# Kernel optimization log

Measured on AMD Instinct MI355X. Metric: run time of the kernel, lower is better.

The kernel has to match this reference:

```python
import jax, jax.numpy as jnp
import numpy as np

NUM_GROUPS = 32
EPS = 1e-6


def group_norm(x, gamma, beta):
    # x: [b, c, h, w]
    b, c, h, w = x.shape
    g = NUM_GROUPS
    xg = x.reshape(b, g, c // g, h, w)
    mean = jnp.mean(xg, axis=(2, 3, 4), keepdims=True)
    var = jnp.var(xg, axis=(2, 3, 4), keepdims=True)
    xg = (xg - mean) * jax.lax.rsqrt(var + EPS)
    x = xg.reshape(b, c, h, w)
    return x * gamma[None, :, None, None] + beta[None, :, None, None]


def conv1x1(x, w, bias):
    # x: [b, c_in, h, w], w: [c_out, c_in], bias: [c_out]
    return jnp.einsum('bihw,oi->bohw', x, w) + bias[None, :, None, None]


def setup_inputs() -> dict:
    key = jax.random.key(0)
    ks = jax.random.split(key, 10)
    c = 512
    b, h, w = 4, 64, 64
    scale = 1.0 / np.sqrt(c)
    inp = {
        'x': jax.random.normal(ks[0], (b, c, h, w), dtype=jnp.float32),
        'gn_gamma': jnp.ones((c,), dtype=jnp.float32),
        'gn_beta': jnp.zeros((c,), dtype=jnp.float32),
        'wq': jax.random.normal(ks[1], (c, c), dtype=jnp.float32) * scale,
        'bq': jnp.zeros((c,), dtype=jnp.float32),
        'wk': jax.random.normal(ks[2], (c, c), dtype=jnp.float32) * scale,
        'bk': jnp.zeros((c,), dtype=jnp.float32),
        'wv': jax.random.normal(ks[3], (c, c), dtype=jnp.float32) * scale,
        'bv': jnp.zeros((c,), dtype=jnp.float32),
        'wo': jax.random.normal(ks[4], (c, c), dtype=jnp.float32) * scale,
        'bo': jnp.zeros((c,), dtype=jnp.float32),
    }
    return inp


def reference(x, gn_gamma, gn_beta, wq, bq, wk, bk, wv, bv, wo, bo):
    b, c, h, w = x.shape
    h_ = group_norm(x, gn_gamma, gn_beta)
    q = conv1x1(h_, wq, bq)
    k = conv1x1(h_, wk, bk)
    v = conv1x1(h_, wv, bv)
    n = h * w
    q = q.reshape(b, c, n).transpose(0, 2, 1)  # [b, n, c]
    k = k.reshape(b, c, n)                      # [b, c, n]
    v = v.reshape(b, c, n).transpose(0, 2, 1)  # [b, n, c]
    sim = jnp.einsum('bqc,bck->bqk', q, k) * (c ** -0.5)  # [b, n, n]
    attn = jax.nn.softmax(sim, axis=-1)
    out = jnp.einsum('bqk,bkc->bqc', attn, v)  # [b, n, c]
    out = out.transpose(0, 2, 1).reshape(b, c, h, w)
    out = conv1x1(out, wo, bo)
    return x + out
```

## Files before the change

kernel.cpp:

```cpp
#include <hip/hip_runtime.h>


typedef __attribute__((ext_vector_type(8))) short bf16x8;
typedef __attribute__((ext_vector_type(4))) float f32x4;

#define MFMA16(a, b, c) __builtin_amdgcn_mfma_f32_16x16x32_bf16((a), (b), (c), 0, 0, 0)

#define B_   4
#define C_   512
#define N_   4096
#define SCALE 0.044194173824159216f
#define ESHIFT 12.0f
#define SC2   0.06376297465050853f
#define ES2   17.312340490667562f

__device__ __forceinline__ unsigned short f2bf(float f) {
    union { float f; unsigned int u; } v; v.f = f;
    unsigned int r = (v.u + 0x7fffu + ((v.u >> 16) & 1u)) >> 16;
    return (unsigned short)r;
}
__device__ __forceinline__ float bf2f(unsigned short s) {
    union { unsigned int u; float f; } v; v.u = ((unsigned int)s) << 16;
    return v.f;
}
// ... 26 lines not shown
    if (t == 0) { part[blk] = red[0]; part[512 + blk] = red[256]; }
}

__global__ __launch_bounds__(256) void gn_apply(const float* __restrict__ x,
                                                const float* __restrict__ gamma,
                                                const float* __restrict__ beta,
                                                const float* __restrict__ part,
                                                unsigned short* __restrict__ ht) {
    __shared__ float tile[64][65];
    __shared__ float mrs[4][2];
    int j0 = blockIdx.x * 64, c0 = blockIdx.y * 64, b = blockIdx.z;
    int t = threadIdx.x;
    if (t < 4) {
        int gid = b * 32 + (c0 >> 4) + t;
        float s = 0.f, ss = 0.f;
#pragma unroll
        for (int q = 0; q < 4; ++q) { s += part[gid * 4 + q]; ss += part[512 + gid * 4 + q]; }
        float mean = s * (1.f / 65536.f);
        float var  = ss * (1.f / 65536.f) - mean * mean;
        mrs[t][0] = mean;
        mrs[t][1] = rsqrtf(var + 1e-6f);
    }
    __syncthreads();
#pragma unroll
    for (int i = 0; i < 16; ++i) {
        int lid = i * 256 + t;
        int cl = lid >> 6, jl = lid & 63;
        int c = c0 + cl;
        float v = x[((size_t)b * C_ + c) * N_ + j0 + jl];
        tile[cl][jl] = (v - mrs[cl >> 4][0]) * mrs[cl >> 4][1] * gamma[c] + beta[c];
    }
    __syncthreads();
#pragma unroll
    for (int i = 0; i < 16; ++i) {
        int lid = i * 256 + t;
        int jl = lid >> 6, cl = lid & 63;
        ht[((size_t)b * N_ + j0 + jl) * C_ + c0 + cl] = f2bf(tile[cl][jl]);
    }
}

__global__ __launch_bounds__(256) void wconv(const float* __restrict__ wq,
                                             const float* __restrict__ wk,
                                             const float* __restrict__ wv,
                                             const float* __restrict__ wo,
                                             unsigned short* __restrict__ dst) {
    size_t i = (size_t)blockIdx.x * 256 + threadIdx.x;
    int m = (int)(i >> 18);
    size_t off = i & 262143;
    const float* src = (m == 0) ? wq : (m == 1) ? wk : (m == 2) ? wv : wo;
    dst[i] = f2bf(src[off]);
}

template <typename EPI>
__device__ __forceinline__ void gemm_core(const unsigned short* __restrict__ Abase,
                                          const unsigned short* __restrict__ Bbase,
                                          size_t lda, size_t ldb, int K, EPI epi) {
    __shared__ unsigned short hl[2][128 * 64];
    __shared__ unsigned short wl[2][128 * 64];
    int t = threadIdx.x;
    int wv = t >> 6, lane = t & 63, l15 = lane & 15, quad = lane >> 4;
    int wm = wv & 1, wn = wv >> 1;
    int srow = lane >> 3;
    int sch  = ((lane & 7) ^ srow) * 8;
    int xr = l15 & 7;
    f32x4 acc[4][4] = {};
#pragma unroll
    for (int i = 0; i < 4; ++i) {
        int seg = wv * 4 + i;
        size_t row = seg * 8 + srow;
        async16(&Abase[row * lda + sch], &hl[0][seg * 512]);
        async16(&Bbase[row * ldb + sch], &wl[0][seg * 512]);
    }
    int nk = K >> 6;
    for (int k = 0; k < nk; ++k) {
        int cur = k & 1;
        __builtin_amdgcn_s_waitcnt(0x3F70);
        __syncthreads();
        if (k + 1 < nk) {
            int k0 = (k + 1) << 6;
#pragma unroll
            for (int i = 0; i < 4; ++i) {
                int seg = wv * 4 + i;
                size_t row = seg * 8 + srow;
                async16(&Abase[row * lda + k0 + sch], &hl[cur ^ 1][seg * 512]);
                async16(&Bbase[row * ldb + k0 + sch], &wl[cur ^ 1][seg * 512]);
            }
        }
#pragma unroll
        for (int kk = 0; kk < 2; ++kk) {
            int sl = (((kk << 2) + quad) ^ xr) * 8;
            bf16x8 af[4], bfr[4];
#pragma unroll
            for (int mi = 0; mi < 4; ++mi)
                af[mi] = *(const bf16x8*)&hl[cur][(wm * 64 + mi * 16 + l15) * 64 + sl];
#pragma unroll
            for (int ni = 0; ni < 4; ++ni)
                bfr[ni] = *(const bf16x8*)&wl[cur][(wn * 64 + ni * 16 + l15) * 64 + sl];
#pragma unroll
            for (int mi = 0; mi < 4; ++mi)
#pragma unroll
                for (int ni = 0; ni < 4; ++ni)
                    acc[mi][ni] = MFMA16(af[mi], bfr[ni], acc[mi][ni]);
        }
    }
    epi(acc, wm, wn, l15, quad);
}

__global__ __launch_bounds__(256) void gemm_qkv(const unsigned short* __restrict__ Ht,
                                                const unsigned short* __restrict__ Wb,
                                                const float* __restrict__ bq,
                                                const float* __restrict__ bk,
                                                const float* __restrict__ bv,
                                                unsigned short* __restrict__ Qt,
                                                unsigned short* __restrict__ Kt,
                                                unsigned short* __restrict__ Vg) {
    int b = blockIdx.z, j0 = blockIdx.x * 128;
    int ct = blockIdx.y;
    int slab = ct >> 2, co0 = (ct & 3) * 128;
    const unsigned short* A = Ht + ((size_t)b * N_ + j0) * C_;
    const unsigned short* B = Wb + (size_t)slab * C_ * C_ + (size_t)co0 * C_;
    const float* bias = (slab == 0) ? bq : (slab == 1) ? bk : bv;
    unsigned short* outqk = (slab == 0) ? Qt : Kt;
    gemm_core(A, B, C_, C_, C_,
        [&](f32x4 (&acc)[4][4], int wm, int wn, int l15, int quad) {
        if (slab < 2) {
#pragma unroll
            for (int mi = 0; mi < 4; ++mi)
#pragma unroll
                for (int ni = 0; ni < 4; ++ni)
#pragma unroll
                    for (int r = 0; r < 4; ++r) {
                        int mrow = wm * 64 + mi * 16 + quad * 4 + r;
                        int ncol = wn * 64 + ni * 16 + l15;
                        outqk[((size_t)b * N_ + j0 + mrow) * C_ + co0 + ncol] =
                            f2bf(acc[mi][ni][r] + bias[co0 + ncol]);
                    }
        } else {
#pragma unroll
            for (int mi = 0; mi < 4; ++mi)
#pragma unroll
                for (int ni = 0; ni < 4; ++ni) {
                    int ncol = wn * 64 + ni * 16 + l15;
                    float bb = bias[co0 + ncol];
                    ushort4 pk;
                    pk.x = f2bf(acc[mi][ni][0] + bb);
                    pk.y = f2bf(acc[mi][ni][1] + bb);
                    pk.z = f2bf(acc[mi][ni][2] + bb);
                    pk.w = f2bf(acc[mi][ni][3] + bb);
                    int jb = j0 + wm * 64 + mi * 16 + quad * 4;
                    *(ushort4*)&Vg[((size_t)b * C_ + co0 + ncol) * N_ + jb] = pk;
                }
        }
    });
}

__global__ __launch_bounds__(512, 4) void gemm_qk_exp(const unsigned short* __restrict__ Qt,
                                                      const unsigned short* __restrict__ Kt,
                                                      unsigned short* __restrict__ P,
                                                      float* __restrict__ psum) {
    extern __shared__ unsigned short sm[];
    int lin = blockIdx.x;
    int xcd = lin & 7;
    int i   = lin >> 3;
    int rid = xcd + 8 * (i >> 4);
    int idx = i & 15;
    int mi4 = idx & 1, ni4 = idx >> 1;
    int b   = rid >> 5;
    int rem = rid & 31;
    int rm  = rem & 7, rn = rem >> 3;
    int j0  = (rm * 2 + mi4) * 256;
    int ky  = rn * 8 + ni4;
    int kc0 = ky * 128;
    const unsigned short* A  = Qt + ((size_t)b * N_ + j0) * C_;
    const unsigned short* Bm = Kt + ((size_t)b * N_ + kc0) * C_;

    int t = threadIdx.x;
    int w = t >> 6, lane = t & 63, l15 = lane & 15, quad = lane >> 4;
    int wm = w >> 1, wn = w & 1;
    int srow = lane >> 2;
    int sch  = ((lane & 3) ^ ((lane >> 3) & 3)) * 8;
    int slotq = (quad ^ ((l15 >> 1) & 3)) * 8;

    const unsigned short* gA0 = A + ((size_t)(w * 2 + 0) * 16 + srow) * C_ + sch;
    const unsigned short* gA1 = A + ((size_t)(w * 2 + 1) * 16 + srow) * C_ + sch;
    const unsigned short* gB  = Bm + ((size_t)w * 16 + srow) * C_ + sch;

    f32x4 acc[4][4] = {};
    const int NT = 16;
    unsigned short* bA = sm;
    unsigned short* bB = sm + 12288;
    unsigned short* bC = sm + 24576;

    async16(gA0,      bA + (w * 2 + 0) * 512);
    async16(gA1,      bA + (w * 2 + 1) * 512);
    async16(gB,       bA + 8192 + w * 512);
    async16(gA0 + 32, bB + (w * 2 + 0) * 512);
    async16(gA1 + 32, bB + (w * 2 + 1) * 512);
    async16(gB  + 32, bB + 8192 + w * 512);
    gA0 += 64; gA1 += 64; gB += 64;
    __builtin_amdgcn_s_waitcnt(0x3F73);
    __builtin_amdgcn_s_barrier();

    for (int tt = 0; tt < NT; ++tt) {
        if (tt + 2 < NT) {
            async16(gA0, bC + (w * 2 + 0) * 512);
            async16(gA1, bC + (w * 2 + 1) * 512);
            async16(gB,  bC + 8192 + w * 512);
            gA0 += 32; gA1 += 32; gB += 32;
        }
        bf16x8 af[4], bfr[4];
#pragma unroll
        for (int mi = 0; mi < 4; ++mi)
            af[mi] = *(const bf16x8*)&bA[(wm * 64 + mi * 16 + l15) * 32 + slotq];
#pragma unroll
        for (int ni = 0; ni < 4; ++ni)
            bfr[ni] = *(const bf16x8*)&bA[8192 + (wn * 64 + ni * 16 + l15) * 32 + slotq];
        __builtin_amdgcn_s_setprio(1);
#pragma unroll
        for (int mi = 0; mi < 4; ++mi)
#pragma unroll
            for (int ni = 0; ni < 4; ++ni)
                acc[mi][ni] = MFMA16(af[mi], bfr[ni], acc[mi][ni]);
        __builtin_amdgcn_s_setprio(0);
        if (tt + 1 < NT) {
            if (tt + 2 < NT) __builtin_amdgcn_s_waitcnt(0x3F73);
            else             __builtin_amdgcn_s_waitcnt(0x3F70);
            __builtin_amdgcn_s_barrier();
        }
        unsigned short* tmp = bA; bA = bB; bB = bC; bC = tmp;
    }

#pragma unroll
    for (int mi = 0; mi < 4; ++mi) {
        float rs[4] = {0.f, 0.f, 0.f, 0.f};
#pragma unroll
        for (int ni = 0; ni < 4; ++ni) {
            int ncol = kc0 + wn * 64 + ni * 16 + l15;
#pragma unroll
            for (int r = 0; r < 4; ++r) {
                int mrow = j0 + wm * 64 + mi * 16 + quad * 4 + r;
                float p = exp2f(__builtin_fmaf(acc[mi][ni][r], SC2, -ES2));
                rs[r] += p;
                P[((size_t)b * N_ + mrow) * N_ + ncol] = f2bf(p);
            }
        }
#pragma unroll
        for (int r = 0; r < 4; ++r) {
            float v = rs[r];
            v += __shfl_xor(v, 1);
            v += __shfl_xor(v, 2);
            v += __shfl_xor(v, 4);
            v += __shfl_xor(v, 8);
            if (l15 == 0)
                psum[(size_t)(ky * 2 + wn) * 16384 +
                     (size_t)b * N_ + j0 + wm * 64 + mi * 16 + quad * 4 + r] = v;
        }
    }
}

__global__ __launch_bounds__(512, 2) void gemm_pv(const unsigned short* __restrict__ P,
                                                  const unsigned short* __restrict__ Vg,
                                                  const float* __restrict__ psum,
                                                  unsigned short* __restrict__ ao) {
    extern __shared__ unsigned short sm[];
    __shared__ float linv[256];
    int lin = blockIdx.x;
    int xcd = lin & 7;
    int i4  = lin >> 3;
    int ct  = i4 & 3;
    int grp = xcd + 8 * (i4 >> 2);
    int b = grp & 3, qtile = grp >> 2;
    int j0 = qtile * 256, co0 = ct * 128;
    int t = threadIdx.x;
    int w = t >> 6, lane = t & 63, l15 = lane & 15, quad = lane >> 4;
    int wm = w >> 1, wn = w & 1;
    int srow = lane >> 2;
    int sch  = ((lane & 3) ^ ((lane >> 3) & 3)) * 8;
    int slotq = (quad ^ ((l15 >> 1) & 3)) * 8;
    const unsigned short* A  = P  + ((size_t)b * N_ + j0) * N_;
    const unsigned short* Bm = Vg + ((size_t)b * C_ + co0) * N_;
    f32x4 acc[4][4] = {};
    const int NT = 128;
#pragma unroll
    for (int tt = 0; tt < 2; ++tt) {
        unsigned short* dst = sm + tt * 12288;
        size_t k0 = (size_t)tt << 5;
#pragma unroll
        for (int i = 0; i < 2; ++i) {
            int seg = w * 2 + i;
            size_t row = (size_t)seg * 16 + srow;
            async16(&A[row * N_ + k0 + sch], dst + seg * 512);
        }
        {
            size_t row = (size_t)w * 16 + srow;
            async16(&Bm[row * N_ + k0 + sch], dst + 8192 + w * 512);
        }
    }
    if (t < 256) {
        size_t q = (size_t)b * N_ + j0 + t;
        float s = 0.f;
#pragma unroll
        for (int i = 0; i < 64; ++i) s += psum[(size_t)i * 16384 + q];
        linv[t] = 1.f / s;
    }
    __builtin_amdgcn_s_waitcnt(0x3F73);
    __builtin_amdgcn_s_barrier();
    for (int tt = 0; tt < NT; tt += 2) {
#pragma unroll
        for (int s = 0; s < 2; ++s) {
            int tc = tt + s;
// ... 2 lines not shown
            bf16x8 af[4], bfr[4];
#pragma unroll
            for (int mi = 0; mi < 4; ++mi)
                af[mi] = *(const bf16x8*)&bp[(wm * 64 + mi * 16 + l15) * 32 + slotq];
#pragma unroll
            for (int ni = 0; ni < 4; ++ni)
                bfr[ni] = *(const bf16x8*)&bp[8192 + (wn * 64 + ni * 16 + l15) * 32 + slotq];
            if (ts < NT) {
                unsigned short* stg = sm + (ts & 3) * 12288;
                size_t k0n = (size_t)ts << 5;
#pragma unroll
                for (int i = 0; i < 2; ++i) {
                    int seg = w * 2 + i;
                    size_t row = (size_t)seg * 16 + srow;
                    async16(&A[row * N_ + k0n + sch], stg + seg * 512);
                }
                {
                    size_t row = (size_t)w * 16 + srow;
                    async16(&Bm[row * N_ + k0n + sch], stg + 8192 + w * 512);
                }
            }
            __builtin_amdgcn_s_setprio(1);
#pragma unroll
            for (int mi = 0; mi < 4; ++mi)
#pragma unroll
                for (int ni = 0; ni < 4; ++ni)
                    acc[mi][ni] = MFMA16(af[mi], bfr[ni], acc[mi][ni]);
            __builtin_amdgcn_s_setprio(0);
            if (s == 0) {
                if (tt + 2 < NT) __builtin_amdgcn_s_waitcnt(0x3F73);
                else             __builtin_amdgcn_s_waitcnt(0x3F70);
                __builtin_amdgcn_sched_barrier(0);
            }
        }
        if (tt + 2 < NT) {
            if (tt + 3 < NT) __builtin_amdgcn_s_waitcnt(0x3F73);
            else             __builtin_amdgcn_s_waitcnt(0x3F70);
            __builtin_amdgcn_s_barrier();
        }
    }
#pragma unroll
    for (int mi = 0; mi < 4; ++mi)
#pragma unroll
        for (int ni = 0; ni < 4; ++ni)
#pragma unroll
            for (int r = 0; r < 4; ++r) {
                int mrow = wm * 64 + mi * 16 + quad * 4 + r;
                int ncol = wn * 64 + ni * 16 + l15;
                ao[((size_t)b * N_ + j0 + mrow) * C_ + co0 + ncol] =
                    f2bf(acc[mi][ni][r] * linv[mrow]);
            }
}

__global__ __launch_bounds__(256) void gemm_resid(const unsigned short* __restrict__ AObf,
                                                  const unsigned short* __restrict__ Wo,
                                                  const float* __restrict__ bo,
                                                  const float* __restrict__ xres,
                                                  float* __restrict__ out) {
    int b = blockIdx.z, j0 = blockIdx.x * 128, co0 = blockIdx.y * 128;
    const unsigned short* A = AObf + ((size_t)b * N_ + j0) * C_;
    const unsigned short* B = Wo + (size_t)co0 * C_;
    gemm_core(A, B, C_, C_, C_,
        [&](f32x4 (&acc)[4][4], int wm, int wn, int l15, int quad) {
#pragma unroll
        for (int mi = 0; mi < 4; ++mi)
#pragma unroll
            for (int ni = 0; ni < 4; ++ni) {
                int ncol = wn * 64 + ni * 16 + l15;
                int jb = j0 + wm * 64 + mi * 16 + quad * 4;
                size_t o = ((size_t)b * C_ + co0 + ncol) * N_ + jb;
                float bb = bo[co0 + ncol];
                float4 xr = *(const float4*)&xres[o];
                float4 ov;
                ov.x = acc[mi][ni][0] + bb + xr.x;
                ov.y = acc[mi][ni][1] + bb + xr.y;
                ov.z = acc[mi][ni][2] + bb + xr.z;
                ov.w = acc[mi][ni][3] + bb + xr.w;
                *(float4*)&out[o] = ov;
            }
    });
}

__global__ __launch_bounds__(256, 1) void flash_attn(const unsigned short* __restrict__ Qt,
                                                     const unsigned short* __restrict__ Kt,
                                                     const unsigned short* __restrict__ Vg,
                                                     unsigned short* __restrict__ part,
                                                     float* __restrict__ lbuf,
                                                     int nsplit) {
    extern __shared__ unsigned short smem[];
    unsigned short* Kl = smem;
    unsigned short* Vl = smem + 32768;
    unsigned short* Pl = smem + 65536;

    int flat = blockIdx.x;
    int qblk, b, s;
    if (nsplit == 2) { s = flat & 1; b = (flat >> 1) & 3; qblk = flat >> 3; }
    else             { s = 0;        b = flat & 3;        qblk = flat >> 2; }
    int q0 = qblk * 128;
    int t = threadIdx.x, w = t >> 6, lane = t & 63, l15 = lane & 15, quad = lane >> 4;
    int klen = N_ / nsplit, kbeg = s * klen, nkt = klen / 32;
    int xr = l15 & 7;

    const unsigned short* Kbase = Kt + (size_t)b * N_ * C_;
    const unsigned short* Vbase = Vg + (size_t)b * C_ * N_;

    bf16x8 qa[2][16];
// ... 122 lines not shown
    size_t row = idx >> 6;
    float l = lbuf[row];
    union { uint4 v; unsigned short u[8]; } p1, p2, outv;
    p1.v = *(const uint4*)&part[row * C_ + cu * 8];
    if (nsplit == 2) {
        l += lbuf[(size_t)B_ * N_ + row];
        p2.v = *(const uint4*)&part[((size_t)B_ * N_ + row) * C_ + cu * 8];
    } else {
        p2.v = make_uint4(0, 0, 0, 0);
    }
    float inv = 1.f / l;
#pragma unroll
    for (int j = 0; j < 8; ++j)
        outv.u[j] = f2bf((bf2f(p1.u[j]) + bf2f(p2.u[j])) * inv);
    *(uint4*)&ao[row * C_ + cu * 8] = outv.v;
}

extern "C" void kernel_launch(void* const* d_in, const int* in_sizes, int n_in,
                              void* d_out, int out_size, void* d_ws, size_t ws_size,
                              hipStream_t stream) {
    const float* x   = (const float*)d_in[0];
    const float* gam = (const float*)d_in[1];
    const float* bet = (const float*)d_in[2];
    const float* wq  = (const float*)d_in[3];
    const float* bq  = (const float*)d_in[4];
    const float* wk  = (const float*)d_in[5];
    const float* bk  = (const float*)d_in[6];
    const float* wv  = (const float*)d_in[7];
    const float* bv  = (const float*)d_in[8];
    const float* wo  = (const float*)d_in[9];
    const float* bo  = (const float*)d_in[10];
    float* out = (float*)d_out;

    char* ws = (char*)d_ws;
    const size_t SZH = (size_t)B_ * N_ * C_ * 2;
    const size_t OFF_HT = 4096;
    const size_t OFF_QT = OFF_HT + SZH;
    const size_t OFF_KT = OFF_QT + SZH;
    const size_t OFF_VG = OFF_KT + SZH;
    const size_t OFF_WB = OFF_VG + SZH;
    const size_t OFF_X  = OFF_WB + 2097152;
    float*          part0 = (float*)ws;
    unsigned short* Ht    = (unsigned short*)(ws + OFF_HT);
    unsigned short* Qt    = (unsigned short*)(ws + OFF_QT);
    unsigned short* Kt    = (unsigned short*)(ws + OFF_KT);
    unsigned short* Vg    = (unsigned short*)(ws + OFF_VG);
    unsigned short* Wb    = (unsigned short*)(ws + OFF_WB);
    unsigned short* AObf  = Ht;

    const size_t SZPSUM = 64ull * 16384 * 4;
    const size_t SZP    = (size_t)B_ * N_ * N_ * 2;
    float*          psum = (float*)(ws + OFF_X);
    unsigned short* P    = (unsigned short*)(ws + OFF_X + SZPSUM);
    size_t needA = OFF_X + SZPSUM + SZP;

    float*          lbuf = (float*)(ws + OFF_X);
    unsigned short* partb = (unsigned short*)(ws + OFF_X + 262144);
    size_t needB2 = OFF_X + 262144 + 2 * SZH;

    gn_partial<<<512, 256, 0, stream>>>(x, part0);
    gn_apply<<<dim3(64, 8, B_), 256, 0, stream>>>(x, gam, bet, part0, Ht);
    wconv<<<4096, 256, 0, stream>>>(wq, wk, wv, wo, Wb);
    gemm_qkv<<<dim3(32, 12, B_), 256, 0, stream>>>(Ht, Wb, bq, bk, bv, Qt, Kt, Vg);

    if (ws_size >= needA) {
        const int QK_LDS = 73728;
        (void)hipFuncSetAttribute((const void*)gemm_qk_exp,
                                  hipFuncAttributeMaxDynamicSharedMemorySize, QK_LDS);
        gemm_qk_exp<<<2048, 512, QK_LDS, stream>>>(Qt, Kt, P, psum);
        const int PV_LDS = 98304;
        (void)hipFuncSetAttribute((const void*)gemm_pv,
                                  hipFuncAttributeMaxDynamicSharedMemorySize, PV_LDS);
        gemm_pv<<<256, 512, PV_LDS, stream>>>(P, Vg, psum, AObf);
    } else {
        int nsplit = (ws_size >= needB2) ? 2 : 1;
        const int FLASH_LDS = 140288;
        (void)hipFuncSetAttribute((const void*)flash_attn,
                                  hipFuncAttributeMaxDynamicSharedMemorySize, FLASH_LDS);
        flash_attn<<<dim3(32 * B_ * nsplit), 256, FLASH_LDS, stream>>>(Qt, Kt, Vg, partb, lbuf, nsplit);
        attn_combine<<<4096, 256, 0, stream>>>(partb, lbuf, AObf, nsplit);
    }
    gemm_resid<<<dim3(32, 4, B_), 256, 0, stream>>>(AObf, Wb + 786432, bo, x, out);
}
```

Baseline: 320.2 us.

## Factor lean triple-buffered GEMM core; use it for QKV and split-K PV

Moves the triple-buffered 256x128 GEMM pipeline from the QK kernel into a shared lean_core helper. The QKV projection now runs on it as a 768-block, 512-thread kernel. PV attention becomes a two-way split-K: partial fp32 outputs are written to workspace, then combined with a separately computed row inverse sum, which raises block count from 256 to 512 for better CU occupancy. The cost is an extra 64MB fp32 partial buffer round trip and two more kernel launches, and the new PV path is used only when the workspace is large enough.

```diff
diff --git a/kernel.cpp b/kernel.cpp
--- a/kernel.cpp
+++ b/kernel.cpp
@@ -102,76 +102,87 @@
 }
 
 template <typename EPI>
-__device__ __forceinline__ void gemm_core(const unsigned short* __restrict__ Abase,
-                                          const unsigned short* __restrict__ Bbase,
-                                          size_t lda, size_t ldb, int K, EPI epi) {
-    __shared__ unsigned short hl[2][128 * 64];
-    __shared__ unsigned short wl[2][128 * 64];
+__device__ __forceinline__ void lean_core(const unsigned short* __restrict__ A,
+                                          const unsigned short* __restrict__ Bm,
+                                          size_t lda, size_t ldb, int NT,
+                                          unsigned short* sm, EPI epi) {
     int t = threadIdx.x;
-    int wv = t >> 6, lane = t & 63, l15 = lane & 15, quad = lane >> 4;
-    int wm = wv & 1, wn = wv >> 1;
-    int srow = lane >> 3;
-    int sch  = ((lane & 7) ^ srow) * 8;
-    int xr = l15 & 7;
+    int w = t >> 6, lane = t & 63, l15 = lane & 15, quad = lane >> 4;
+    int wm = w >> 1, wn = w & 1;
+    int srow = lane >> 2;
+    int sch  = ((lane & 3) ^ ((lane >> 3) & 3)) * 8;
+    int slotq = (quad ^ ((l15 >> 1) & 3)) * 8;
+
+    const unsigned short* gA0 = A + ((size_t)(w * 2 + 0) * 16 + srow) * lda + sch;
+    const unsigned short* gA1 = A + ((size_t)(w * 2 + 1) * 16 + srow) * lda + sch;
+    const unsigned short* gB  = Bm + ((size_t)w * 16 + srow) * ldb + sch;
+
     f32x4 acc[4][4] = {};
-#pragma unroll
-    for (int i = 0; i < 4; ++i) {
-        int seg = wv * 4 + i;
-        size_t row = seg * 8 + srow;
-        async16(&Abase[row * lda + sch], &hl[0][seg * 512]);
-        async16(&Bbase[row * ldb + sch], &wl[0][seg * 512]);
-    }
-    int nk = K >> 6;
-    for (int k = 0; k < nk; ++k) {
-        int cur = k & 1;
-        __builtin_amdgcn_s_waitcnt(0x3F70);
-        __syncthreads();
-        if (k + 1 < nk) {
-            int k0 = (k + 1) << 6;
-#pragma unroll
-            for (int i = 0; i < 4; ++i) {
-                int seg = wv * 4 + i;
-                size_t row = seg * 8 + srow;
-                async16(&Abase[row * lda + k0 + sch], &hl[cur ^ 1][seg * 512]);
-                async16(&Bbase[row * ldb + k0 + sch], &wl[cur ^ 1][seg * 512]);
-            }
-        }
-#pragma unroll
-        for (int kk = 0; kk < 2; ++kk) {
-            int sl = (((kk << 2) + quad) ^ xr) * 8;
-            bf16x8 af[4], bfr[4];
-#pragma unroll
-            for (int mi = 0; mi < 4; ++mi)
-                af[mi] = *(const bf16x8*)&hl[cur][(wm * 64 + mi * 16 + l15) * 64 + sl];
+    unsigned short* bA = sm;
+    unsigned short* bB = sm + 12288;
+    unsigned short* bC = sm + 24576;
+
+    async16(gA0,      bA + (w * 2 + 0) * 512);
+    async16(gA1,      bA + (w * 2 + 1) * 512);
+    async16(gB,       bA + 8192 + w * 512);
+    async16(gA0 + 32, bB + (w * 2 + 0) * 512);
+    async16(gA1 + 32, bB + (w * 2 + 1) * 512);
+    async16(gB  + 32, bB + 8192 + w * 512);
+    gA0 += 64; gA1 += 64; gB += 64;
+    __builtin_amdgcn_s_waitcnt(0x3F73);
+    __builtin_amdgcn_s_barrier();
+
+    for (int tt = 0; tt < NT; ++tt) {
+        if (tt + 2 < NT) {
+            async16(gA0, bC + (w * 2 + 0) * 512);
+            async16(gA1, bC + (w * 2 + 1) * 512);
+            async16(gB,  bC + 8192 + w * 512);
+            gA0 += 32; gA1 += 32; gB += 32;
+        }
+        bf16x8 af[4], bfr[4];
+#pragma unroll
+        for (int mi = 0; mi < 4; ++mi)
+            af[mi] = *(const bf16x8*)&bA[(wm * 64 + mi * 16 + l15) * 32 + slotq];
+#pragma unroll
+        for (int ni = 0; ni < 4; ++ni)
+            bfr[ni] = *(const bf16x8*)&bA[8192 + (wn * 64 + ni * 16 + l15) * 32 + slotq];
+        __builtin_amdgcn_s_setprio(1);
+#pragma unroll
+        for (int mi = 0; mi < 4; ++mi)
 #pragma unroll
             for (int ni = 0; ni < 4; ++ni)
-                bfr[ni] = *(const bf16x8*)&wl[cur][(wn * 64 + ni * 16 + l15) * 64 + sl];
-#pragma unroll
-            for (int mi = 0; mi < 4; ++mi)
-#pragma unroll
-                for (int ni = 0; ni < 4; ++ni)
-                    acc[mi][ni] = MFMA16(af[mi], bfr[ni], acc[mi][ni]);
-        }
+                acc[mi][ni] = MFMA16(af[mi], bfr[ni], acc[mi][ni]);
+        __builtin_amdgcn_s_setprio(0);
+        if (tt + 1 < NT) {
+            if (tt + 2 < NT) __builtin_amdgcn_s_waitcnt(0x3F73);
+            else             __builtin_amdgcn_s_waitcnt(0x3F70);
+            __builtin_amdgcn_s_barrier();
+        }
+        unsigned short* tmp = bA; bA = bB; bB = bC; bC = tmp;
     }
     epi(acc, wm, wn, l15, quad);
 }
 
-__global__ __launch_bounds__(256) void gemm_qkv(const unsigned short* __restrict__ Ht,
-                                                const unsigned short* __restrict__ Wb,
-                                                const float* __restrict__ bq,
-                                                const float* __restrict__ bk,
-                                                const float* __restrict__ bv,
-                                                unsigned short* __restrict__ Qt,
-                                                unsigned short* __restrict__ Kt,
-                                                unsigned short* __restrict__ Vg) {
-    int b = blockIdx.z, j0 = blockIdx.x * 128;
-    int ct = blockIdx.y;
-    int slab = ct >> 2, co0 = (ct & 3) * 128;
+__global__ __launch_bounds__(512, 4) void gemm_qkv2(const unsigned short* __restrict__ Ht,
+                                                    const unsigned short* __restrict__ Wb,
+                                                    const float* __restrict__ bq,
+                                                    const float* __restrict__ bk,
+                                                    const float* __restrict__ bv,
+                                                    unsigned short* __restrict__ Qt,
+                                                    unsigned short* __restrict__ Kt,
+                                                    unsigned short* __restrict__ Vg) {
+    extern __shared__ unsigned short sm[];
+    int lin = blockIdx.x;
+    int slab = lin % 3;
+    int q    = lin / 3;
+    int b  = q & 3;
+    int ct = (q >> 2) & 3, jt = q >> 4;
+    int j0 = jt * 256, co0 = ct * 128;
     const unsigned short* A = Ht + ((size_t)b * N_ + j0) * C_;
     const unsigned short* B = Wb + (size_t)slab * C_ * C_ + (size_t)co0 * C_;
     const float* bias = (slab == 0) ? bq : (slab == 1) ? bk : bv;
     unsigned short* outqk = (slab == 0) ? Qt : Kt;
-    gemm_core(A, B, C_, C_, C_,
+    lean_core(A, B, C_, C_, 16, sm,
         [&](f32x4 (&acc)[4][4], int wm, int wn, int l15, int quad) {
         if (slab < 2) {
 #pragma unroll
@@ -223,89 +234,89 @@
     int kc0 = ky * 128;
     const unsigned short* A  = Qt + ((size_t)b * N_ + j0) * C_;
     const unsigned short* Bm = Kt + ((size_t)b * N_ + kc0) * C_;
-
-    int t = threadIdx.x;
-    int w = t >> 6, lane = t & 63, l15 = lane & 15, quad = lane >> 4;
-    int wm = w >> 1, wn = w & 1;
-    int srow = lane >> 2;
-    int sch  = ((lane & 3) ^ ((lane >> 3) & 3)) * 8;
-    int slotq = (quad ^ ((l15 >> 1) & 3)) * 8;
-
-    const unsigned short* gA0 = A + ((size_t)(w * 2 + 0) * 16 + srow) * C_ + sch;
-    const unsigned short* gA1 = A + ((size_t)(w * 2 + 1) * 16 + srow) * C_ + sch;
-    const unsigned short* gB  = Bm + ((size_t)w * 16 + srow) * C_ + sch;
-
-    f32x4 acc[4][4] = {};
-    const int NT = 16;
-    unsigned short* bA = sm;
-    unsigned short* bB = sm + 12288;
-    unsigned short* bC = sm + 24576;
-
-    async16(gA0,      bA + (w * 2 + 0) * 512);
-    async16(gA1,      bA + (w * 2 + 1) * 512);
-    async16(gB,       bA + 8192 + w * 512);
-    async16(gA0 + 32, bB + (w * 2 + 0) * 512);
-    async16(gA1 + 32, bB + (w * 2 + 1) * 512);
-    async16(gB  + 32, bB + 8192 + w * 512);
-    gA0 += 64; gA1 += 64; gB += 64;
-    __builtin_amdgcn_s_waitcnt(0x3F73);
-    __builtin_amdgcn_s_barrier();
-
-    for (int tt = 0; tt < NT; ++tt) {
-        if (tt + 2 < NT) {
-            async16(gA0, bC + (w * 2 + 0) * 512);
-            async16(gA1, bC + (w * 2 + 1) * 512);
-            async16(gB,  bC + 8192 + w * 512);
-            gA0 += 32; gA1 += 32; gB += 32;
-        }
-        bf16x8 af[4], bfr[4];
+    lean_core(A, Bm, C_, C_, 16, sm,
+        [&](f32x4 (&acc)[4][4], int wm, int wn, int l15, int quad) {
+#pragma unroll
+        for (int mi = 0; mi < 4; ++mi) {
+            float rs[4] = {0.f, 0.f, 0.f, 0.f};
+#pragma unroll
+            for (int ni = 0; ni < 4; ++ni) {
+                int ncol = kc0 + wn * 64 + ni * 16 + l15;
+#pragma unroll
+                for (int r = 0; r < 4; ++r) {
+                    int mrow = j0 + wm * 64 + mi * 16 + quad * 4 + r;
+                    float p = exp2f(__builtin_fmaf(acc[mi][ni][r], SC2, -ES2));
+                    rs[r] += p;
+                    P[((size_t)b * N_ + mrow) * N_ + ncol] = f2bf(p);
+                }
+            }
+#pragma unroll
+            for (int r = 0; r < 4; ++r) {
+                float v = rs[r];
+                v += __shfl_xor(v, 1);
+                v += __shfl_xor(v, 2);
+                v += __shfl_xor(v, 4);
+                v += __shfl_xor(v, 8);
+                if (l15 == 0)
+                    psum[(size_t)(ky * 2 + wn) * 16384 +
+                         (size_t)b * N_ + j0 + wm * 64 + mi * 16 + quad * 4 + r] = v;
+            }
+        }
+    });
+}
+
+__global__ __launch_bounds__(512, 4) void pv_part(const unsigned short* __restrict__ P,
+                                                  const unsigned short* __restrict__ Vg,
+                                                  float* __restrict__ opart) {
+    extern __shared__ unsigned short sm[];
+    int lin = blockIdx.x;
+    int ks  = lin >> 8;
+    int r   = lin & 255;
+    int b = r & 3, qtile = (r >> 2) & 15, ct = r >> 6;
+    int j0 = qtile * 256, co0 = ct * 128;
+    const unsigned short* A  = P  + ((size_t)b * N_ + j0) * N_ + (size_t)ks * 2048;
+    const unsigned short* Bm = Vg + ((size_t)b * C_ + co0) * N_ + (size_t)ks * 2048;
+    lean_core(A, Bm, N_, N_, 64, sm,
+        [&](f32x4 (&acc)[4][4], int wm, int wn, int l15, int quad) {
 #pragma unroll
         for (int mi = 0; mi < 4; ++mi)
-            af[mi] = *(const bf16x8*)&bA[(wm * 64 + mi * 16 + l15) * 32 + slotq];
-#pragma unroll
-        for (int ni = 0; ni < 4; ++ni)
-            bfr[ni] = *(const bf16x8*)&bA[8192 + (wn * 64 + ni * 16 + l15) * 32 + slotq];
-        __builtin_amdgcn_s_setprio(1);
-#pragma unroll
-        for (int mi = 0; mi < 4; ++mi)
 #pragma unroll
             for (int ni = 0; ni < 4; ++ni)
-                acc[mi][ni] = MFMA16(af[mi], bfr[ni], acc[mi][ni]);
-        __builtin_amdgcn_s_setprio(0);
-        if (tt + 1 < NT) {
-            if (tt + 2 < NT) __builtin_amdgcn_s_waitcnt(0x3F73);
-            else             __builtin_amdgcn_s_waitcnt(0x3F70);
-            __builtin_amdgcn_s_barrier();
-        }
-        unsigned short* tmp = bA; bA = bB; bB = bC; bC = tmp;
-    }
-
-#pragma unroll
-    for (int mi = 0; mi < 4; ++mi) {
-        float rs[4] = {0.f, 0.f, 0.f, 0.f};
-#pragma unroll
-        for (int ni = 0; ni < 4; ++ni) {
-            int ncol = kc0 + wn * 64 + ni * 16 + l15;
-#pragma unroll
-            for (int r = 0; r < 4; ++r) {
-                int mrow = j0 + wm * 64 + mi * 16 + quad * 4 + r;
-                float p = exp2f(__builtin_fmaf(acc[mi][ni][r], SC2, -ES2));
-                rs[r] += p;
-                P[((size_t)b * N_ + mrow) * N_ + ncol] = f2bf(p);
-            }
-        }
-#pragma unroll
-        for (int r = 0; r < 4; ++r) {
-            float v = rs[r];
-            v += __shfl_xor(v, 1);
-            v += __shfl_xor(v, 2);
-            v += __shfl_xor(v, 4);
-            v += __shfl_xor(v, 8);
-            if (l15 == 0)
-                psum[(size_t)(ky * 2 + wn) * 16384 +
-                     (size_t)b * N_ + j0 + wm * 64 + mi * 16 + quad * 4 + r] = v;
-        }
-    }
+#pragma unroll
+                for (int r2 = 0; r2 < 4; ++r2) {
+                    int mrow = wm * 64 + mi * 16 + quad * 4 + r2;
+                    int ncol = wn * 64 + ni * 16 + l15;
+                    opart[((size_t)ks * 16384 + (size_t)b * N_ + j0 + mrow) * C_ +
+                          co0 + ncol] = acc[mi][ni][r2];
+                }
+    });
+}
+
+__global__ __launch_bounds__(256) void pv_linv(const float* __restrict__ psum,
+                                               float* __restrict__ linv) {
+    int q = blockIdx.x * 256 + threadIdx.x;
+    float s = 0.f;
+#pragma unroll
+    for (int i = 0; i < 64; ++i) s += psum[(size_t)i * 16384 + q];
+    linv[q] = 1.f / s;
+}
+
+__global__ __launch_bounds__(256) void pv_comb(const float* __restrict__ part,
+                                               const float* __restrict__ linv,
+                                               unsigned short* __restrict__ ao) {
+    size_t idx = (size_t)blockIdx.x * 256 + threadIdx.x;
+    size_t row = idx >> 7;
+    int c4 = (int)(idx & 127) * 4;
+    size_t o = row * C_ + c4;
+    float4 p0 = *(const float4*)&part[o];
+    float4 p1 = *(const float4*)&part[(size_t)16384 * C_ + o];
+    float inv = linv[row];
+    ushort4 rv;
+    rv.x = f2bf((p0.x + p1.x) * inv);
+    rv.y = f2bf((p0.y + p1.y) * inv);
+    rv.z = f2bf((p0.z + p1.z) * inv);
+    rv.w = f2bf((p0.w + p1.w) * inv);
+    *(ushort4*)&ao[o] = rv;
 }
 
 __global__ __launch_bounds__(512, 2) void gemm_pv(const unsigned short* __restrict__ P,
@@ -414,6 +425,61 @@
             }
 }
 
+template <typename EPI>
+__device__ __forceinline__ void gemm_core(const unsigned short* __restrict__ Abase,
+                                          const unsigned short* __restrict__ Bbase,
+                                          size_t lda, size_t ldb, int K, EPI epi) {
+    __shared__ unsigned short hl[2][128 * 64];
+    __shared__ unsigned short wl[2][128 * 64];
+    int t = threadIdx.x;
+    int wv = t >> 6, lane = t & 63, l15 = lane & 15, quad = lane >> 4;
+    int wm = wv & 1, wn = wv >> 1;
+    int srow = lane >> 3;
+    int sch  = ((lane & 7) ^ srow) * 8;
+    int xr = l15 & 7;
+    f32x4 acc[4][4] = {};
+#pragma unroll
+    for (int i = 0; i < 4; ++i) {
+        int seg = wv * 4 + i;
+        size_t row = seg * 8 + srow;
+        async16(&Abase[row * lda + sch], &hl[0][seg * 512]);
+        async16(&Bbase[row * ldb + sch], &wl[0][seg * 512]);
+    }
+    int nk = K >> 6;
+    for (int k = 0; k < nk; ++k) {
+        int cur = k & 1;
+        __builtin_amdgcn_s_waitcnt(0x3F70);
+        __syncthreads();
+        if (k + 1 < nk) {
+            int k0 = (k + 1) << 6;
+#pragma unroll
+            for (int i = 0; i < 4; ++i) {
+                int seg = wv * 4 + i;
+                size_t row = seg * 8 + srow;
+                async16(&Abase[row * lda + k0 + sch], &hl[cur ^ 1][seg * 512]);
+                async16(&Bbase[row * ldb + k0 + sch], &wl[cur ^ 1][seg * 512]);
+            }
+        }
+#pragma unroll
+        for (int kk = 0; kk < 2; ++kk) {
+            int sl = (((kk << 2) + quad) ^ xr) * 8;
+            bf16x8 af[4], bfr[4];
+#pragma unroll
+            for (int mi = 0; mi < 4; ++mi)
+                af[mi] = *(const bf16x8*)&hl[cur][(wm * 64 + mi * 16 + l15) * 64 + sl];
+#pragma unroll
+            for (int ni = 0; ni < 4; ++ni)
+                bfr[ni] = *(const bf16x8*)&wl[cur][(wn * 64 + ni * 16 + l15) * 64 + sl];
+#pragma unroll
+            for (int mi = 0; mi < 4; ++mi)
+#pragma unroll
+                for (int ni = 0; ni < 4; ++ni)
+                    acc[mi][ni] = MFMA16(af[mi], bfr[ni], acc[mi][ni]);
+        }
+    }
+    epi(acc, wm, wn, l15, quad);
+}
+
 __global__ __launch_bounds__(256) void gemm_resid(const unsigned short* __restrict__ AObf,
                                                   const unsigned short* __restrict__ Wo,
                                                   const float* __restrict__ bo,
@@ -642,26 +708,40 @@
     const size_t SZP    = (size_t)B_ * N_ * N_ * 2;
     float*          psum = (float*)(ws + OFF_X);
     unsigned short* P    = (unsigned short*)(ws + OFF_X + SZPSUM);
-    size_t needA = OFF_X + SZPSUM + SZP;
+    size_t needA  = OFF_X + SZPSUM + SZP;
+    float* opart = (float*)(ws + needA);
+    float* linvb = (float*)(ws + needA + 67108864ull);
+    size_t needA2 = needA + 67108864ull + 65536ull;
 
     float*          lbuf = (float*)(ws + OFF_X);
     unsigned short* partb = (unsigned short*)(ws + OFF_X + 262144);
     size_t needB2 = OFF_X + 262144 + 2 * SZH;
 
+    const int LEAN_LDS = 73728;
+
     gn_partial<<<512, 256, 0, stream>>>(x, part0);
     gn_apply<<<dim3(64, 8, B_), 256, 0, stream>>>(x, gam, bet, part0, Ht);
     wconv<<<4096, 256, 0, stream>>>(wq, wk, wv, wo, Wb);
-    gemm_qkv<<<dim3(32, 12, B_), 256, 0, stream>>>(Ht, Wb, bq, bk, bv, Qt, Kt, Vg);
+    (void)hipFuncSetAttribute((const void*)gemm_qkv2,
+                              hipFuncAttributeMaxDynamicSharedMemorySize, LEAN_LDS);
+    gemm_qkv2<<<768, 512, LEAN_LDS, stream>>>(Ht, Wb, bq, bk, bv, Qt, Kt, Vg);
 
     if (ws_size >= needA) {
-        const int QK_LDS = 73728;
         (void)hipFuncSetAttribute((const void*)gemm_qk_exp,
-                                  hipFuncAttributeMaxDynamicSharedMemorySize, QK_LDS);
-        gemm_qk_exp<<<2048, 512, QK_LDS, stream>>>(Qt, Kt, P, psum);
-        const int PV_LDS = 98304;
-        (void)hipFuncSetAttribute((const void*)gemm_pv,
-                                  hipFuncAttributeMaxDynamicSharedMemorySize, PV_LDS);
-        gemm_pv<<<256, 512, PV_LDS, stream>>>(P, Vg, psum, AObf);
+                                  hipFuncAttributeMaxDynamicSharedMemorySize, LEAN_LDS);
+        gemm_qk_exp<<<2048, 512, LEAN_LDS, stream>>>(Qt, Kt, P, psum);
+        if (ws_size >= needA2) {
+            pv_linv<<<64, 256, 0, stream>>>(psum, linvb);
+            (void)hipFuncSetAttribute((const void*)pv_part,
+                                      hipFuncAttributeMaxDynamicSharedMemorySize, LEAN_LDS);
+            pv_part<<<512, 512, LEAN_LDS, stream>>>(P, Vg, opart);
+            pv_comb<<<8192, 256, 0, stream>>>(opart, linvb, AObf);
+        } else {
+            const int PV_LDS = 98304;
+            (void)hipFuncSetAttribute((const void*)gemm_pv,
+                                      hipFuncAttributeMaxDynamicSharedMemorySize, PV_LDS);
+            gemm_pv<<<256, 512, PV_LDS, stream>>>(P, Vg, psum, AObf);
+        }
     } else {
         int nsplit = (ws_size >= needB2) ? 2 : 1;
         const int FLASH_LDS = 140288;
```

Result: no change. 325.2 us (+1.6%).

## Load QK B operand directly to registers and reuse lean pipeline for QKV GEMM

Applied to the files above, without the earlier changes.

Moves the triple-buffered lean GEMM loop into a shared helper and uses it in a new 512-thread QKV projection kernel with 256x128 tiles and a slab-interleaved block order. For the QK^T+exp kernel, a variant now fetches the K operand straight from global memory into registers each k-step instead of staging it in LDS, which cuts LDS use from 72KB to 48KB and may allow higher occupancy. The cost is that global-load latency for B now sits on the critical path every iteration, with no prefetch ahead of the MFMAs.

```diff
diff --git a/kernel.cpp b/kernel.cpp
--- a/kernel.cpp
+++ b/kernel.cpp
@@ -102,76 +102,149 @@
 }
 
 template <typename EPI>
-__device__ __forceinline__ void gemm_core(const unsigned short* __restrict__ Abase,
-                                          const unsigned short* __restrict__ Bbase,
-                                          size_t lda, size_t ldb, int K, EPI epi) {
-    __shared__ unsigned short hl[2][128 * 64];
-    __shared__ unsigned short wl[2][128 * 64];
+__device__ __forceinline__ void lean_core(const unsigned short* __restrict__ A,
+                                          const unsigned short* __restrict__ Bm,
+                                          size_t lda, size_t ldb, int NT,
+                                          unsigned short* sm, EPI epi) {
     int t = threadIdx.x;
-    int wv = t >> 6, lane = t & 63, l15 = lane & 15, quad = lane >> 4;
-    int wm = wv & 1, wn = wv >> 1;
-    int srow = lane >> 3;
-    int sch  = ((lane & 7) ^ srow) * 8;
-    int xr = l15 & 7;
+    int w = t >> 6, lane = t & 63, l15 = lane & 15, quad = lane >> 4;
+    int wm = w >> 1, wn = w & 1;
+    int srow = lane >> 2;
+    int sch  = ((lane & 3) ^ ((lane >> 3) & 3)) * 8;
+    int slotq = (quad ^ ((l15 >> 1) & 3)) * 8;
+
+    const unsigned short* gA0 = A + ((size_t)(w * 2 + 0) * 16 + srow) * lda + sch;
+    const unsigned short* gA1 = A + ((size_t)(w * 2 + 1) * 16 + srow) * lda + sch;
+    const unsigned short* gB  = Bm + ((size_t)w * 16 + srow) * ldb + sch;
+
     f32x4 acc[4][4] = {};
-#pragma unroll
-    for (int i = 0; i < 4; ++i) {
-        int seg = wv * 4 + i;
-        size_t row = seg * 8 + srow;
-        async16(&Abase[row * lda + sch], &hl[0][seg * 512]);
-        async16(&Bbase[row * ldb + sch], &wl[0][seg * 512]);
-    }
-    int nk = K >> 6;
-    for (int k = 0; k < nk; ++k) {
-        int cur = k & 1;
-        __builtin_amdgcn_s_waitcnt(0x3F70);
-        __syncthreads();
-        if (k + 1 < nk) {
-            int k0 = (k + 1) << 6;
-#pragma unroll
-            for (int i = 0; i < 4; ++i) {
-                int seg = wv * 4 + i;
-                size_t row = seg * 8 + srow;
-                async16(&Abase[row * lda + k0 + sch], &hl[cur ^ 1][seg * 512]);
-                async16(&Bbase[row * ldb + k0 + sch], &wl[cur ^ 1][seg * 512]);
-            }
-        }
-#pragma unroll
-        for (int kk = 0; kk < 2; ++kk) {
-            int sl = (((kk << 2) + quad) ^ xr) * 8;
-            bf16x8 af[4], bfr[4];
-#pragma unroll
-            for (int mi = 0; mi < 4; ++mi)
-                af[mi] = *(const bf16x8*)&hl[cur][(wm * 64 + mi * 16 + l15) * 64 + sl];
+    unsigned short* bA = sm;
+    unsigned short* bB = sm + 12288;
+    unsigned short* bC = sm + 24576;
+
+    async16(gA0,      bA + (w * 2 + 0) * 512);
+    async16(gA1,      bA + (w * 2 + 1) * 512);
+    async16(gB,       bA + 8192 + w * 512);
+    async16(gA0 + 32, bB + (w * 2 + 0) * 512);
+    async16(gA1 + 32, bB + (w * 2 + 1) * 512);
+    async16(gB  + 32, bB + 8192 + w * 512);
+    gA0 += 64; gA1 += 64; gB += 64;
+    __builtin_amdgcn_s_waitcnt(0x3F73);
+    __builtin_amdgcn_s_barrier();
+
+    for (int tt = 0; tt < NT; ++tt) {
+        if (tt + 2 < NT) {
+            async16(gA0, bC + (w * 2 + 0) * 512);
+            async16(gA1, bC + (w * 2 + 1) * 512);
+            async16(gB,  bC + 8192 + w * 512);
+            gA0 += 32; gA1 += 32; gB += 32;
+        }
+        bf16x8 af[4], bfr[4];
+#pragma unroll
+        for (int mi = 0; mi < 4; ++mi)
+            af[mi] = *(const bf16x8*)&bA[(wm * 64 + mi * 16 + l15) * 32 + slotq];
+#pragma unroll
+        for (int ni = 0; ni < 4; ++ni)
+            bfr[ni] = *(const bf16x8*)&bA[8192 + (wn * 64 + ni * 16 + l15) * 32 + slotq];
+        __builtin_amdgcn_s_setprio(1);
+#pragma unroll
+        for (int mi = 0; mi < 4; ++mi)
 #pragma unroll
             for (int ni = 0; ni < 4; ++ni)
-                bfr[ni] = *(const bf16x8*)&wl[cur][(wn * 64 + ni * 16 + l15) * 64 + sl];
-#pragma unroll
-            for (int mi = 0; mi < 4; ++mi)
-#pragma unroll
-                for (int ni = 0; ni < 4; ++ni)
-                    acc[mi][ni] = MFMA16(af[mi], bfr[ni], acc[mi][ni]);
-        }
+                acc[mi][ni] = MFMA16(af[mi], bfr[ni], acc[mi][ni]);
+        __builtin_amdgcn_s_setprio(0);
+        if (tt + 1 < NT) {
+            if (tt + 2 < NT) __builtin_amdgcn_s_waitcnt(0x3F73);
+            else             __builtin_amdgcn_s_waitcnt(0x3F70);
+            __builtin_amdgcn_s_barrier();
+        }
+        unsigned short* tmp = bA; bA = bB; bB = bC; bC = tmp;
     }
     epi(acc, wm, wn, l15, quad);
 }
 
-__global__ __launch_bounds__(256) void gemm_qkv(const unsigned short* __restrict__ Ht,
-                                                const unsigned short* __restrict__ Wb,
-                                                const float* __restrict__ bq,
-                                                const float* __restrict__ bk,
-                                                const float* __restrict__ bv,
-                                                unsigned short* __restrict__ Qt,
-                                                unsigned short* __restrict__ Kt,
-                                                unsigned short* __restrict__ Vg) {
-    int b = blockIdx.z, j0 = blockIdx.x * 128;
-    int ct = blockIdx.y;
-    int slab = ct >> 2, co0 = (ct & 3) * 128;
+template <typename EPI>
+__device__ __forceinline__ void lean_bd(const unsigned short* __restrict__ A,
+                                        const unsigned short* __restrict__ Bm,
+                                        size_t lda, size_t ldb, int NT,
+                                        unsigned short* sm, EPI epi) {
+    int t = threadIdx.x;
+    int w = t >> 6, lane = t & 63, l15 = lane & 15, quad = lane >> 4;
+    int wm = w >> 1, wn = w & 1;
+    int srow = lane >> 2;
+    int sch  = ((lane & 3) ^ ((lane >> 3) & 3)) * 8;
+    int slotq = (quad ^ ((l15 >> 1) & 3)) * 8;
+
+    const unsigned short* gA0 = A + ((size_t)(w * 2 + 0) * 16 + srow) * lda + sch;
+    const unsigned short* gA1 = A + ((size_t)(w * 2 + 1) * 16 + srow) * lda + sch;
+    const unsigned short* gB  = Bm + ((size_t)(wn * 64 + l15)) * ldb + quad * 8;
+
+    f32x4 acc[4][4] = {};
+    unsigned short* bA = sm;
+    unsigned short* bB = sm + 8192;
+    unsigned short* bC = sm + 16384;
+
+    async16(gA0,      bA + (w * 2 + 0) * 512);
+    async16(gA1,      bA + (w * 2 + 1) * 512);
+    async16(gA0 + 32, bB + (w * 2 + 0) * 512);
+    async16(gA1 + 32, bB + (w * 2 + 1) * 512);
+    gA0 += 64; gA1 += 64;
+    __builtin_amdgcn_s_waitcnt(0x3F70);
+    __builtin_amdgcn_sched_barrier(0);
+    __builtin_amdgcn_s_barrier();
+
+    for (int tt = 0; tt < NT; ++tt) {
+        bf16x8 bcur[4];
+#pragma unroll
+        for (int ni = 0; ni < 4; ++ni)
+            bcur[ni] = *(const bf16x8*)(gB + (size_t)ni * 16 * ldb);
+        gB += 32;
+        if (tt + 2 < NT) {
+            async16(gA0, bC + (w * 2 + 0) * 512);
+            async16(gA1, bC + (w * 2 + 1) * 512);
+            gA0 += 32; gA1 += 32;
+        }
+        bf16x8 af[4];
+#pragma unroll
+        for (int mi = 0; mi < 4; ++mi)
+            af[mi] = *(const bf16x8*)&bA[(wm * 64 + mi * 16 + l15) * 32 + slotq];
+        __builtin_amdgcn_s_setprio(1);
+#pragma unroll
+        for (int mi = 0; mi < 4; ++mi)
+#pragma unroll
+            for (int ni = 0; ni < 4; ++ni)
+                acc[mi][ni] = MFMA16(af[mi], bcur[ni], acc[mi][ni]);
+        __builtin_amdgcn_s_setprio(0);
+        if (tt + 1 < NT) {
+            __builtin_amdgcn_s_waitcnt(0x3F70);
+            __builtin_amdgcn_sched_barrier(0);
+            __builtin_amdgcn_s_barrier();
+        }
+        unsigned short* tmp = bA; bA = bB; bB = bC; bC = tmp;
+    }
+    epi(acc, wm, wn, l15, quad);
+}
+
+__global__ __launch_bounds__(512, 4) void gemm_qkv2(const unsigned short* __restrict__ Ht,
+                                                    const unsigned short* __restrict__ Wb,
+                                                    const float* __restrict__ bq,
+                                                    const float* __restrict__ bk,
+                                                    const float* __restrict__ bv,
+                                                    unsigned short* __restrict__ Qt,
+                                                    unsigned short* __restrict__ Kt,
+                                                    unsigned short* __restrict__ Vg) {
+    extern __shared__ unsigned short sm[];
+    int lin = blockIdx.x;
+    int slab = lin % 3;
+    int q    = lin / 3;
+    int b  = q & 3;
+    int ct = (q >> 2) & 3, jt = q >> 4;
+    int j0 = jt * 256, co0 = ct * 128;
     const unsigned short* A = Ht + ((size_t)b * N_ + j0) * C_;
     const unsigned short* B = Wb + (size_t)slab * C_ * C_ + (size_t)co0 * C_;
     const float* bias = (slab == 0) ? bq : (slab == 1) ? bk : bv;
     unsigned short* outqk = (slab == 0) ? Qt : Kt;
-    gemm_core(A, B, C_, C_, C_,
+    lean_core(A, B, C_, C_, 16, sm,
         [&](f32x4 (&acc)[4][4], int wm, int wn, int l15, int quad) {
         if (slab < 2) {
 #pragma unroll
@@ -223,89 +296,35 @@
     int kc0 = ky * 128;
     const unsigned short* A  = Qt + ((size_t)b * N_ + j0) * C_;
     const unsigned short* Bm = Kt + ((size_t)b * N_ + kc0) * C_;
-
-    int t = threadIdx.x;
-    int w = t >> 6, lane = t & 63, l15 = lane & 15, quad = lane >> 4;
-    int wm = w >> 1, wn = w & 1;
-    int srow = lane >> 2;
-    int sch  = ((lane & 3) ^ ((lane >> 3) & 3)) * 8;
-    int slotq = (quad ^ ((l15 >> 1) & 3)) * 8;
-
-    const unsigned short* gA0 = A + ((size_t)(w * 2 + 0) * 16 + srow) * C_ + sch;
-    const unsigned short* gA1 = A + ((size_t)(w * 2 + 1) * 16 + srow) * C_ + sch;
-    const unsigned short* gB  = Bm + ((size_t)w * 16 + srow) * C_ + sch;
-
-    f32x4 acc[4][4] = {};
-    const int NT = 16;
-    unsigned short* bA = sm;
-    unsigned short* bB = sm + 12288;
-    unsigned short* bC = sm + 24576;
-
-    async16(gA0,      bA + (w * 2 + 0) * 512);
-    async16(gA1,      bA + (w * 2 + 1) * 512);
-    async16(gB,       bA + 8192 + w * 512);
-    async16(gA0 + 32, bB + (w * 2 + 0) * 512);
-    async16(gA1 + 32, bB + (w * 2 + 1) * 512);
-    async16(gB  + 32, bB + 8192 + w * 512);
-    gA0 += 64; gA1 += 64; gB += 64;
-    __builtin_amdgcn_s_waitcnt(0x3F73);
-    __builtin_amdgcn_s_barrier();
-
-    for (int tt = 0; tt < NT; ++tt) {
-        if (tt + 2 < NT) {
-            async16(gA0, bC + (w * 2 + 0) * 512);
-            async16(gA1, bC + (w * 2 + 1) * 512);
-            async16(gB,  bC + 8192 + w * 512);
-            gA0 += 32; gA1 += 32; gB += 32;
-        }
-        bf16x8 af[4], bfr[4];
-#pragma unroll
-        for (int mi = 0; mi < 4; ++mi)
-            af[mi] = *(const bf16x8*)&bA[(wm * 64 + mi * 16 + l15) * 32 + slotq];
-#pragma unroll
-        for (int ni = 0; ni < 4; ++ni)
-            bfr[ni] = *(const bf16x8*)&bA[8192 + (wn * 64 + ni * 16 + l15) * 32 + slotq];
-        __builtin_amdgcn_s_setprio(1);
-#pragma unroll
-        for (int mi = 0; mi < 4; ++mi)
-#pragma unroll
-            for (int ni = 0; ni < 4; ++ni)
-                acc[mi][ni] = MFMA16(af[mi], bfr[ni], acc[mi][ni]);
-        __builtin_amdgcn_s_setprio(0);
-        if (tt + 1 < NT) {
-            if (tt + 2 < NT) __builtin_amdgcn_s_waitcnt(0x3F73);
-            else             __builtin_amdgcn_s_waitcnt(0x3F70);
-            __builtin_amdgcn_s_barrier();
-        }
-        unsigned short* tmp = bA; bA = bB; bB = bC; bC = tmp;
-    }
-
-#pragma unroll
-    for (int mi = 0; mi < 4; ++mi) {
-        float rs[4] = {0.f, 0.f, 0.f, 0.f};
-#pragma unroll
-        for (int ni = 0; ni < 4; ++ni) {
-            int ncol = kc0 + wn * 64 + ni * 16 + l15;
+    lean_bd(A, Bm, C_, C_, 16, sm,
+        [&](f32x4 (&acc)[4][4], int wm, int wn, int l15, int quad) {
+#pragma unroll
+        for (int mi = 0; mi < 4; ++mi) {
+            float rs[4] = {0.f, 0.f, 0.f, 0.f};
+#pragma unroll
+            for (int ni = 0; ni < 4; ++ni) {
+                int ncol = kc0 + wn * 64 + ni * 16 + l15;
+#pragma unroll
+                for (int r = 0; r < 4; ++r) {
+                    int mrow = j0 + wm * 64 + mi * 16 + quad * 4 + r;
+                    float p = exp2f(__builtin_fmaf(acc[mi][ni][r], SC2, -ES2));
+                    rs[r] += p;
+                    P[((size_t)b * N_ + mrow) * N_ + ncol] = f2bf(p);
+                }
+            }
 #pragma unroll
             for (int r = 0; r < 4; ++r) {
-                int mrow = j0 + wm * 64 + mi * 16 + quad * 4 + r;
-                float p = exp2f(__builtin_fmaf(acc[mi][ni][r], SC2, -ES2));
-                rs[r] += p;
-                P[((size_t)b * N_ + mrow) * N_ + ncol] = f2bf(p);
-            }
-        }
-#pragma unroll
-        for (int r = 0; r < 4; ++r) {
-            float v = rs[r];
-            v += __shfl_xor(v, 1);
-            v += __shfl_xor(v, 2);
-            v += __shfl_xor(v, 4);
-            v += __shfl_xor(v, 8);
-            if (l15 == 0)
-                psum[(size_t)(ky * 2 + wn) * 16384 +
-                     (size_t)b * N_ + j0 + wm * 64 + mi * 16 + quad * 4 + r] = v;
-        }
-    }
+                float v = rs[r];
+                v += __shfl_xor(v, 1);
+                v += __shfl_xor(v, 2);
+                v += __shfl_xor(v, 4);
+                v += __shfl_xor(v, 8);
+                if (l15 == 0)
+                    psum[(size_t)(ky * 2 + wn) * 16384 +
+                         (size_t)b * N_ + j0 + wm * 64 + mi * 16 + quad * 4 + r] = v;
+            }
+        }
+    });
 }
 
 __global__ __launch_bounds__(512, 2) void gemm_pv(const unsigned short* __restrict__ P,
@@ -414,6 +433,61 @@
             }
 }
 
+template <typename EPI>
+__device__ __forceinline__ void gemm_core(const unsigned short* __restrict__ Abase,
+                                          const unsigned short* __restrict__ Bbase,
+                                          size_t lda, size_t ldb, int K, EPI epi) {
+    __shared__ unsigned short hl[2][128 * 64];
+    __shared__ unsigned short wl[2][128 * 64];
+    int t = threadIdx.x;
+    int wv = t >> 6, lane = t & 63, l15 = lane & 15, quad = lane >> 4;
+    int wm = wv & 1, wn = wv >> 1;
+    int srow = lane >> 3;
+    int sch  = ((lane & 7) ^ srow) * 8;
+    int xr = l15 & 7;
+    f32x4 acc[4][4] = {};
+#pragma unroll
+    for (int i = 0; i < 4; ++i) {
+        int seg = wv * 4 + i;
+        size_t row = seg * 8 + srow;
+        async16(&Abase[row * lda + sch], &hl[0][seg * 512]);
+        async16(&Bbase[row * ldb + sch], &wl[0][seg * 512]);
+    }
+    int nk = K >> 6;
+    for (int k = 0; k < nk; ++k) {
+        int cur = k & 1;
+        __builtin_amdgcn_s_waitcnt(0x3F70);
+        __syncthreads();
+        if (k + 1 < nk) {
+            int k0 = (k + 1) << 6;
+#pragma unroll
+            for (int i = 0; i < 4; ++i) {
+                int seg = wv * 4 + i;
+                size_t row = seg * 8 + srow;
+                async16(&Abase[row * lda + k0 + sch], &hl[cur ^ 1][seg * 512]);
+                async16(&Bbase[row * ldb + k0 + sch], &wl[cur ^ 1][seg * 512]);
+            }
+        }
+#pragma unroll
+        for (int kk = 0; kk < 2; ++kk) {
+            int sl = (((kk << 2) + quad) ^ xr) * 8;
+            bf16x8 af[4], bfr[4];
+#pragma unroll
+            for (int mi = 0; mi < 4; ++mi)
+                af[mi] = *(const bf16x8*)&hl[cur][(wm * 64 + mi * 16 + l15) * 64 + sl];
+#pragma unroll
+            for (int ni = 0; ni < 4; ++ni)
+                bfr[ni] = *(const bf16x8*)&wl[cur][(wn * 64 + ni * 16 + l15) * 64 + sl];
+#pragma unroll
+            for (int mi = 0; mi < 4; ++mi)
+#pragma unroll
+                for (int ni = 0; ni < 4; ++ni)
+                    acc[mi][ni] = MFMA16(af[mi], bfr[ni], acc[mi][ni]);
+        }
+    }
+    epi(acc, wm, wn, l15, quad);
+}
+
 __global__ __launch_bounds__(256) void gemm_resid(const unsigned short* __restrict__ AObf,
                                                   const unsigned short* __restrict__ Wo,
                                                   const float* __restrict__ bo,
@@ -642,22 +716,26 @@
     const size_t SZP    = (size_t)B_ * N_ * N_ * 2;
     float*          psum = (float*)(ws + OFF_X);
     unsigned short* P    = (unsigned short*)(ws + OFF_X + SZPSUM);
-    size_t needA = OFF_X + SZPSUM + SZP;
+    size_t needA  = OFF_X + SZPSUM + SZP;
 
     float*          lbuf = (float*)(ws + OFF_X);
     unsigned short* partb = (unsigned short*)(ws + OFF_X + 262144);
     size_t needB2 = OFF_X + 262144 + 2 * SZH;
 
+    const int LEAN_LDS = 73728;
+    const int BD_LDS   = 49152;
+
     gn_partial<<<512, 256, 0, stream>>>(x, part0);
     gn_apply<<<dim3(64, 8, B_), 256, 0, stream>>>(x, gam, bet, part0, Ht);
     wconv<<<4096, 256, 0, stream>>>(wq, wk, wv, wo, Wb);
-    gemm_qkv<<<dim3(32, 12, B_), 256, 0, stream>>>(Ht, Wb, bq, bk, bv, Qt, Kt, Vg);
+    (void)hipFuncSetAttribute((const void*)gemm_qkv2,
+                              hipFuncAttributeMaxDynamicSharedMemorySize, LEAN_LDS);
+    gemm_qkv2<<<768, 512, LEAN_LDS, stream>>>(Ht, Wb, bq, bk, bv, Qt, Kt, Vg);
 
     if (ws_size >= needA) {
-        const int QK_LDS = 73728;
         (void)hipFuncSetAttribute((const void*)gemm_qk_exp,
-                                  hipFuncAttributeMaxDynamicSharedMemorySize, QK_LDS);
-        gemm_qk_exp<<<2048, 512, QK_LDS, stream>>>(Qt, Kt, P, psum);
+                                  hipFuncAttributeMaxDynamicSharedMemorySize, BD_LDS);
+        gemm_qk_exp<<<2048, 512, BD_LDS, stream>>>(Qt, Kt, P, psum);
         const int PV_LDS = 98304;
         (void)hipFuncSetAttribute((const void*)gemm_pv,
                                   hipFuncAttributeMaxDynamicSharedMemorySize, PV_LDS);
```

Measured after the change: 400.3 us. 25.0% more time.
